# Kernel optimization log

Measured on AMD Instinct MI355X. Metric: run time of the kernel, lower is better.

Reference implementation:

```python
import jax, jax.numpy as jnp
import numpy as np

LAMBDA_DEPTHG = 0.3
STEGO_TEMPERATURE = 0.1
KNN_K = 7
DEPTH_SIGMA = 0.5
EPS = 1e-8


def _l2norm(x):
    return x / jnp.sqrt(jnp.sum(x * x, axis=-1, keepdims=True) + EPS)


def _stego_loss(codes, feats, temperature, knn_k):
    # Pairwise cosine similarity of DINO features -> KNN graph (includes self).
    f = _l2norm(feats)                                  # (B,N,Df)
    sim_f = jnp.einsum('bnd,bmd->bnm', f, f)            # (B,N,N)
    _, knn_idx = jax.lax.top_k(sim_f, knn_k)            # (B,N,k) int32
    # Temperature-scaled InfoNCE over code similarities; KNN entries are positives.
    c = _l2norm(codes)                                  # (B,N,Dc)
    logits = jnp.einsum('bnd,bmd->bnm', c, c) / temperature  # (B,N,N)
    logp = jax.nn.log_softmax(logits, axis=-1)          # (B,N,N)
    pos_logp = jnp.take_along_axis(logp, knn_idx, axis=-1)   # (B,N,k)
    return -jnp.mean(pos_logp)


def _depth_guided_correlation_loss(codes, depth, sigma_d):
    # Gaussian depth affinity: pixels at similar depth should have similar codes.
    dd = depth[:, :, None] - depth[:, None, :]          # (B,N,N)
    w = jnp.exp(-(dd * dd) / (2.0 * sigma_d * sigma_d)) # (B,N,N)
    c = _l2norm(codes)
    s = jnp.einsum('bnd,bmd->bnm', c, c)                # (B,N,N) cosine corr
    return jnp.mean(w * (1.0 - s))


def setup_inputs() -> dict:
    key = jax.random.key(0)
    k1, k2, k3 = jax.random.split(key, 3)
    B, N = 2, 4096
    semantic_codes = jax.random.normal(k1, (B, N, 90), dtype=jnp.float32)
    dino_features = jax.random.normal(k2, (B, N, 384), dtype=jnp.float32)
    depth = jax.random.uniform(k3, (B, N), dtype=jnp.float32)
    return {"semantic_codes": semantic_codes, "dino_features": dino_features, "depth": depth}


def reference(semantic_codes, dino_features, depth):
    l_stego = _stego_loss(semantic_codes, dino_features, STEGO_TEMPERATURE, KNN_K)
    l_depthg = _depth_guided_correlation_loss(semantic_codes, depth, DEPTH_SIGMA)
    total = l_stego + LAMBDA_DEPTHG * l_depthg
    return (l_stego, l_depthg, total)
```

## Files before the change

### kernel.cpp

```cpp
#include <hip/hip_runtime.h>
#include <math.h>

#define NPTS 4096

typedef __attribute__((ext_vector_type(8))) short bf16x8;
typedef __attribute__((ext_vector_type(16))) float f32x16;
typedef long fp8x8;

#define KEEP(x) asm volatile("" : "+v"(x))

__device__ __forceinline__ f32x16 zero16() {
  f32x16 z;
#pragma unroll
  for (int i = 0; i < 16; ++i) z[i] = 0.f;
  return z;
}

__device__ __forceinline__ unsigned packkey(float x, int m) {
  unsigned u = __float_as_uint(x);
  unsigned key = u ^ ((unsigned)((int)u >> 31) | 0x80000000u);
  return (key & 0xFFFFF000u) | (unsigned)m;
}

__device__ __forceinline__ void cas7(unsigned v, unsigned* s) {
#pragma unroll
  for (int t = 0; t < 7; ++t) {
    const unsigned hi = s[t] >= v ? s[t] : v;
    const unsigned lo = s[t] >= v ? v : s[t];
    s[t] = hi;
    v = lo;
  }
}

#define KSENT 0u

__device__ __forceinline__ unsigned bf16pack(float a, float b) {
  unsigned ua = __float_as_uint(a); ua = (ua + 0x7FFFu + ((ua >> 16) & 1u)) >> 16;
  unsigned ub = __float_as_uint(b); ub = (ub + 0x7FFFu + ((ub >> 16) & 1u)) >> 16;
  return ua | (ub << 16);
}

__global__ __launch_bounds__(64) void norm_all(const float* __restrict__ feats,
                                               const float* __restrict__ codes,
                                               unsigned char* __restrict__ Fsw8,
                                               unsigned short* __restrict__ Csw,
                                               float* __restrict__ invc) {
  const int row = blockIdx.x;
  const int lane = threadIdx.x;
  const int b = row >> 12, mt = (row >> 5) & 127, rl = row & 31;

  const float* f = feats + (size_t)row * 384;
  float v[8];
  float ss = 0.f;
  if (lane < 48) {
    float4 p0 = *(const float4*)(f + lane * 8);
    float4 p1 = *(const float4*)(f + lane * 8 + 4);
    v[0] = p0.x; v[1] = p0.y; v[2] = p0.z; v[3] = p0.w;
    v[4] = p1.x; v[5] = p1.y; v[6] = p1.z; v[7] = p1.w;
#pragma unroll
    for (int e = 0; e < 8; ++e) ss = fmaf(v[e], v[e], ss);
  }
#pragma unroll
  for (int m = 1; m <= 32; m <<= 1) ss += __shfl_xor(ss, m, 64);
  const float s8 = rsqrtf(ss + 1e-8f) * 8.0f;
  if (lane < 48) {
    int w0 = __builtin_amdgcn_cvt_pk_fp8_f32(v[0] * s8, v[1] * s8, 0, 0);
    w0 = __builtin_amdgcn_cvt_pk_fp8_f32(v[2] * s8, v[3] * s8, w0, 1);
    int w1 = __builtin_amdgcn_cvt_pk_fp8_f32(v[4] * s8, v[5] * s8, 0, 0);
    w1 = __builtin_amdgcn_cvt_pk_fp8_f32(v[6] * s8, v[7] * s8, w1, 1);
    const int kc = lane >> 1, hs = lane & 1;
    uint2 o = make_uint2((unsigned)w0, (unsigned)w1);
    *(uint2*)(Fsw8 + (((size_t)(b * 128 + mt) * 24 + kc) << 9) + (hs * 32 + rl) * 8) = o;
  }

  const float* c = codes + (size_t)row * 90;
  float cv[8];
#pragma unroll
  for (int e = 0; e < 8; ++e) cv[e] = 0.f;
  if (lane < 11) {
    float4 p0 = *(const float4*)(c + lane * 8);
    float4 p1 = *(const float4*)(c + lane * 8 + 4);
    cv[0] = p0.x; cv[1] = p0.y; cv[2] = p0.z; cv[3] = p0.w;
    cv[4] = p1.x; cv[5] = p1.y; cv[6] = p1.z; cv[7] = p1.w;
  } else if (lane == 11) {
    cv[0] = c[88]; cv[1] = c[89];
  }
  float cs = 0.f;
#pragma unroll
  for (int e = 0; e < 8; ++e) cs = fmaf(cv[e], cv[e], cs);
#pragma unroll
  for (int m = 1; m <= 32; m <<= 1) cs += __shfl_xor(cs, m, 64);
  const float cinv = rsqrtf(cs + 1e-8f);
  if (lane < 12) {
    uint4 o;
    o.x = bf16pack(cv[0] * cinv, cv[1] * cinv);
    o.y = bf16pack(cv[2] * cinv, cv[3] * cinv);
    o.z = bf16pack(cv[4] * cinv, cv[5] * cinv);
    o.w = bf16pack(cv[6] * cinv, cv[7] * cinv);
    const int kc = lane >> 1, hs = lane & 1;
    *(uint4*)(Csw + (((size_t)(b * 128 + mt) * 6 + kc) << 9) + (hs * 32 + rl) * 8) = o;
  }
  if (lane == 0) invc[row] = cinv;
}

__global__ __launch_bounds__(1024, 1) void knn_mfma(const unsigned char* __restrict__ Fsw8,
                                                    unsigned* __restrict__ cand) {
  __shared__ unsigned ckey[16][32][7];
  const int g = blockIdx.x;
  const int b = g & 1;
  const int qt = g >> 1;
  const int q0 = qt * 32;
  const int tid = threadIdx.x;
  const int w = tid >> 6;
  const int lane = tid & 63;
  const int lo = lane & 31, hi4 = (lane >> 5) * 4;
  const unsigned char* Fb = Fsw8 + (size_t)b * 128 * 24 * 512;

  fp8x8 bfr[24];
  {
    const unsigned char* qb = Fb + ((size_t)qt * 24) * 512 + lane * 8;
#pragma unroll
    for (int t = 0; t < 24; ++t) bfr[t] = *(const fp8x8*)(qb + t * 512);
#pragma unroll
    for (int t = 0; t < 24; ++t) KEEP(bfr[t]);
  }
  unsigned s7[7];
#pragma unroll
  for (int t = 0; t < 7; ++t) s7[t] = KSENT;

  const int t0 = w * 8;
  const unsigned char* ab = Fb + ((size_t)t0 * 24) * 512 + lane * 8;

  fp8x8 a[12];
  for (int mt = 0; mt < 8; ++mt) {
    const unsigned char* art = ab + (size_t)mt * 24 * 512;
    f32x16 acc = zero16();
#pragma unroll
    for (int t = 0; t < 12; ++t) a[t] = *(const fp8x8*)(art + t * 512);
#pragma unroll
    for (int t = 0; t < 12; ++t) KEEP(a[t]);
#pragma unroll
    for (int t = 0; t < 12; ++t)
      acc = __builtin_amdgcn_mfma_f32_32x32x16_fp8_fp8(a[t], bfr[t], acc, 0, 0, 0);
#pragma unroll
    for (int t = 0; t < 12; ++t) a[t] = *(const fp8x8*)(art + (12 + t) * 512);
#pragma unroll
    for (int t = 0; t < 12; ++t) KEEP(a[t]);
#pragma unroll
    for (int t = 0; t < 12; ++t)
      acc = __builtin_amdgcn_mfma_f32_32x32x16_fp8_fp8(a[t], bfr[12 + t], acc, 0, 0, 0);
    const int mb = (t0 + mt) * 32 + hi4;
#pragma unroll
    for (int r = 0; r < 16; ++r) {
      const int m = mb + (r & 3) + 8 * (r >> 2);
      cas7(packkey(acc[r], m), s7);
    }
  }

#pragma unroll
  for (int t = 0; t < 7; ++t) {
    const unsigned ov = (unsigned)__shfl_xor((int)s7[t], 32, 64);
    cas7(ov, s7);
  }
  if (lane < 32) {
#pragma unroll
    for (int t = 0; t < 7; ++t) ckey[w][lo][t] = s7[t];
  }
  __syncthreads();

  if (tid < 32) {
    unsigned fs[7];
#pragma unroll
    for (int t = 0; t < 7; ++t) fs[t] = KSENT;
    for (int w2 = 0; w2 < 16; ++w2)
#pragma unroll
      for (int t = 0; t < 7; ++t) cas7(ckey[w2][tid][t], fs);
    unsigned* o = cand + ((size_t)(b * NPTS) + q0 + tid) * 7;
#pragma unroll
    for (int t = 0; t < 7; ++t) o[t] = fs[t];
  }
}

__global__ __launch_bounds__(512, 1) void lse_depth(const unsigned short* __restrict__ Csw,
                                                    const float* __restrict__ depth,
                                                    float* __restrict__ slse_part,
                                                    float* __restrict__ dpart) {
  __shared__ float lsep[8][32];
  __shared__ float depp[8];
  const int g = blockIdx.x;
  const int b = g & 1;
  const int h = (g >> 1) & 1;
  const int qt = g >> 2;
  const int q0 = qt * 32;
  const int tid = threadIdx.x;
  const int w = tid >> 6;
  const int lane = tid & 63;
  const int lo = lane & 31, hi4 = (lane >> 5) * 4;
  const unsigned short* Cb = Csw + (size_t)b * 128 * 6 * 512;
  const float* db = depth + b * NPTS;

  bf16x8 bfr[6];
  {
    const unsigned short* qb = Cb + ((size_t)qt * 6) * 512 + lane * 8;
#pragma unroll
    for (int t = 0; t < 6; ++t) bfr[t] = *(const bf16x8*)(qb + t * 512);
#pragma unroll
    for (int t = 0; t < 6; ++t) KEEP(bfr[t]);
  }
  const float dq = db[q0 + lo];
  float slse = 0.f, sdep = 0.f;

  const int t0 = h * 64 + w * 8;
  const unsigned short* ab = Cb + ((size_t)t0 * 6) * 512 + lane * 8;

  bf16x8 a0[6], a1[6];
#pragma unroll
  for (int t = 0; t < 6; ++t) a0[t] = *(const bf16x8*)(ab + t * 512);
#pragma unroll
  for (int t = 0; t < 6; ++t) KEEP(a0[t]);

#define PROC3(A, GT)                                                           \
  {                                                                            \
    f32x16 acc = zero16();                                                     \
    _Pragma("unroll")                                                          \
    for (int t = 0; t < 6; ++t)                                                \
      acc = __builtin_amdgcn_mfma_f32_32x32x16_bf16(A[t], bfr[t], acc, 0, 0, 0); \
    float dvv[16];                                                             \
    _Pragma("unroll")                                                          \
    for (int k = 0; k < 4; ++k) {                                              \
      float4 dv = *(const float4*)(db + (GT) * 32 + hi4 + 8 * k);              \
      dvv[k * 4 + 0] = dv.x; dvv[k * 4 + 1] = dv.y;                            \
      dvv[k * 4 + 2] = dv.z; dvv[k * 4 + 3] = dv.w;                            \
    }                                                                          \
    _Pragma("unroll")                                                          \
    for (int r = 0; r < 16; ++r) {                                             \
      const float s = acc[r];                                                  \
      const float dd = dq - dvv[r];                                            \
      sdep += __expf(-2.f * dd * dd) * (1.f - s);                              \
      slse += __expf(fmaf(s, 10.f, -10.f));                                    \
    }                                                                          \
  }

  for (int mt = 0; mt < 8; mt += 2) {
    {
      const unsigned short* ar = ab + (size_t)(mt + 1) * 6 * 512;
#pragma unroll
      for (int t = 0; t < 6; ++t) a1[t] = *(const bf16x8*)(ar + t * 512);
#pragma unroll
      for (int t = 0; t < 6; ++t) KEEP(a1[t]);
    }
    PROC3(a0, t0 + mt)
    if (mt + 2 < 8) {
      const unsigned short* ar = ab + (size_t)(mt + 2) * 6 * 512;
#pragma unroll
      for (int t = 0; t < 6; ++t) a0[t] = *(const bf16x8*)(ar + t * 512);
#pragma unroll
      for (int t = 0; t < 6; ++t) KEEP(a0[t]);
    }
    PROC3(a1, t0 + mt + 1)
  }
#undef PROC3

  slse += __shfl_xor(slse, 32, 64);
  if (lane < 32) lsep[w][lo] = slse;
#pragma unroll
  for (int m = 1; m <= 32; m <<= 1) sdep += __shfl_xor(sdep, m, 64);
  if (lane == 0) depp[w] = sdep;
  __syncthreads();
  if (tid < 32) {
    float tot = 0.f;
#pragma unroll
    for (int w2 = 0; w2 < 8; ++w2) tot += lsep[w2][tid];
    slse_part[(size_t)((h * 2 + b) * NPTS) + q0 + tid] = tot;
  }
  if (tid == 32) {
    float d = 0.f;
#pragma unroll
    for (int w2 = 0; w2 < 8; ++w2) d += depp[w2];
    dpart[g] = d;
  }
}

__global__ __launch_bounds__(64) void gather_pos(const float* __restrict__ codes,
                                                 const float* __restrict__ invc,
                                                 const unsigned* __restrict__ cand,
                                                 float* __restrict__ gpart) {
  const int n = blockIdx.x;
  const int b = n >> 12, q = n & 4095;
  const int lane = threadIdx.x;

  unsigned s[7];
  const unsigned* cp = cand + (size_t)n * 7;
#pragma unroll
  for (int t = 0; t < 7; ++t) s[t] = cp[t];
  bool has = false;
#pragma unroll
  for (int t = 0; t < 7; ++t) has = has || ((s[t] & 4095u) == (unsigned)q);
  if (!has) s[6] = (unsigned)q;

  const float* cn = codes + (size_t)n * 90;
  float2 a = make_float2(0.f, 0.f);
  if (lane < 45) a = *(const float2*)(cn + lane * 2);
  const float inva = invc[n];
  float ssum = 0.f;
#pragma unroll
  for (int k = 0; k < 7; ++k) {
    const int m = (int)(s[k] & 4095u);
    const float* cm = codes + ((size_t)(b << 12) + m) * 90;
    float2 bb = make_float2(0.f, 0.f);
    if (lane < 45) bb = *(const float2*)(cm + lane * 2);
    float p = fmaf(a.x, bb.x, a.y * bb.y);
#pragma unroll
    for (int w = 1; w <= 32; w <<= 1) p += __shfl_xor(p, w, 64);
    ssum += p * inva * invc[(b << 12) + m];
  }
  if (lane == 0) gpart[n] = ssum;
}

__global__ __launch_bounds__(256) void finalize(const float* __restrict__ slse_part,
                                                const float* __restrict__ gpart,
                                                const float* __restrict__ dpart,
                                                float* __restrict__ out) {
  const int tid = threadIdx.x;
  float s1 = 0.f, s2 = 0.f;
  for (int n = tid; n < 2 * NPTS; n += 256) {
    const int b = n >> 12, q = n & 4095;
    const float pz = slse_part[b * NPTS + q] + slse_part[(2 + b) * NPTS + q];
    s1 += 10.f + __logf(pz);
    s2 += gpart[n];
  }
  float s3 = dpart[tid] + dpart[tid + 256];
  __shared__ float r1[256], r2[256], r3[256];
  r1[tid] = s1; r2[tid] = s2; r3[tid] = s3;
  __syncthreads();
  for (int s = 128; s > 0; s >>= 1) {
    if (tid < s) { r1[tid] += r1[tid + s]; r2[tid] += r2[tid + s]; r3[tid] += r3[tid + s]; }
    __syncthreads();
  }
  if (tid == 0) {
    const float l_st = (7.f * r1[0] - 10.f * r2[0]) / 57344.f;
    const float l_dp = r3[0] / 33554432.f;
    out[0] = l_st;
    out[1] = l_dp;
    out[2] = l_st + 0.3f * l_dp;
  }
}

extern "C" void kernel_launch(void* const* d_in, const int* in_sizes, int n_in,
                              void* d_out, int out_size, void* d_ws, size_t ws_size,
                              hipStream_t stream) {
  (void)in_sizes; (void)n_in; (void)out_size; (void)ws_size;
  const float* codes = (const float*)d_in[0];
  const float* feats = (const float*)d_in[1];
  const float* depth = (const float*)d_in[2];
  float* out = (float*)d_out;

  char* ws = (char*)d_ws;
  float*    invc      = (float*)ws;
  unsigned* cand      = (unsigned*)(ws + 32768);
  unsigned char*  Fsw8 = (unsigned char*)(ws + 262144);
  unsigned short* Csw  = (unsigned short*)(ws + 3407872);
  float*    slse_part = (float*)(ws + 4980736);
  float*    dpart     = (float*)(ws + 5046272);
  float*    gpart     = (float*)(ws + 5048320);

  norm_all<<<2 * NPTS, 64, 0, stream>>>(feats, codes, Fsw8, Csw, invc);
  knn_mfma<<<256, 1024, 0, stream>>>(Fsw8, cand);
  lse_depth<<<512, 512, 0, stream>>>(Csw, depth, slse_part, dpart);
  gather_pos<<<2 * NPTS, 64, 0, stream>>>(codes, invc, cand, gpart);
  finalize<<<1, 256, 0, stream>>>(slse_part, gpart, dpart, out);
}
```

Before: 89.76 us.

## Stage KNN query fragments in LDS, double-buffer key loads, merge LSE halves

In the KNN kernel the 24 query fp8 fragments now go into shared memory instead of staying pinned in registers, and the key-tile loads are double-buffered so the next tile's first half is fetched while the current MFMAs run. This frees VGPRs and hides global load latency, at the cost of LDS reads on every iteration. Separately, lse_depth now runs 1024 threads per block across all 128 key tiles, so each query's full sum is done in one block and the log is taken there. That removes the split-half partials and simplifies finalize, but halves the grid to 256 blocks.

```diff
diff --git a/kernel.cpp b/kernel.cpp
--- a/kernel.cpp
+++ b/kernel.cpp
@@ -105,6 +105,7 @@
 
 __global__ __launch_bounds__(1024, 1) void knn_mfma(const unsigned char* __restrict__ Fsw8,
                                                     unsigned* __restrict__ cand) {
+  __shared__ unsigned long long qfrag[24 * 64];
   __shared__ unsigned ckey[16][32][7];
   const int g = blockIdx.x;
   const int b = g & 1;
@@ -116,14 +117,17 @@
   const int lo = lane & 31, hi4 = (lane >> 5) * 4;
   const unsigned char* Fb = Fsw8 + (size_t)b * 128 * 24 * 512;
 
-  fp8x8 bfr[24];
   {
-    const unsigned char* qb = Fb + ((size_t)qt * 24) * 512 + lane * 8;
-#pragma unroll
-    for (int t = 0; t < 24; ++t) bfr[t] = *(const fp8x8*)(qb + t * 512);
-#pragma unroll
-    for (int t = 0; t < 24; ++t) KEEP(bfr[t]);
-  }
+    const unsigned long long* src =
+        (const unsigned long long*)(Fb + ((size_t)qt * 24) * 512);
+#pragma unroll
+    for (int k = 0; k < 2; ++k) {
+      const int i = tid + k * 1024;
+      if (i < 24 * 64) qfrag[i] = src[i];
+    }
+  }
+  __syncthreads();
+
   unsigned s7[7];
 #pragma unroll
   for (int t = 0; t < 7; ++t) s7[t] = KSENT;
@@ -131,24 +135,40 @@
   const int t0 = w * 8;
   const unsigned char* ab = Fb + ((size_t)t0 * 24) * 512 + lane * 8;
 
-  fp8x8 a[12];
+  fp8x8 a0[12], a1[12], bq[12];
+#pragma unroll
+  for (int t = 0; t < 12; ++t) a0[t] = *(const fp8x8*)(ab + t * 512);
+#pragma unroll
+  for (int t = 0; t < 12; ++t) KEEP(a0[t]);
+
   for (int mt = 0; mt < 8; ++mt) {
     const unsigned char* art = ab + (size_t)mt * 24 * 512;
+#pragma unroll
+    for (int t = 0; t < 12; ++t) a1[t] = *(const fp8x8*)(art + (12 + t) * 512);
+#pragma unroll
+    for (int t = 0; t < 12; ++t) KEEP(a1[t]);
+#pragma unroll
+    for (int t = 0; t < 12; ++t) bq[t] = (fp8x8)qfrag[t * 64 + lane];
+#pragma unroll
+    for (int t = 0; t < 12; ++t) KEEP(bq[t]);
     f32x16 acc = zero16();
 #pragma unroll
-    for (int t = 0; t < 12; ++t) a[t] = *(const fp8x8*)(art + t * 512);
-#pragma unroll
-    for (int t = 0; t < 12; ++t) KEEP(a[t]);
-#pragma unroll
     for (int t = 0; t < 12; ++t)
-      acc = __builtin_amdgcn_mfma_f32_32x32x16_fp8_fp8(a[t], bfr[t], acc, 0, 0, 0);
-#pragma unroll
-    for (int t = 0; t < 12; ++t) a[t] = *(const fp8x8*)(art + (12 + t) * 512);
-#pragma unroll
-    for (int t = 0; t < 12; ++t) KEEP(a[t]);
+      acc = __builtin_amdgcn_mfma_f32_32x32x16_fp8_fp8(a0[t], bq[t], acc, 0, 0, 0);
+    if (mt + 1 < 8) {
+      const unsigned char* arn = ab + (size_t)(mt + 1) * 24 * 512;
+#pragma unroll
+      for (int t = 0; t < 12; ++t) a0[t] = *(const fp8x8*)(arn + t * 512);
+#pragma unroll
+      for (int t = 0; t < 12; ++t) KEEP(a0[t]);
+    }
+#pragma unroll
+    for (int t = 0; t < 12; ++t) bq[t] = (fp8x8)qfrag[(12 + t) * 64 + lane];
+#pragma unroll
+    for (int t = 0; t < 12; ++t) KEEP(bq[t]);
 #pragma unroll
     for (int t = 0; t < 12; ++t)
-      acc = __builtin_amdgcn_mfma_f32_32x32x16_fp8_fp8(a[t], bfr[12 + t], acc, 0, 0, 0);
+      acc = __builtin_amdgcn_mfma_f32_32x32x16_fp8_fp8(a1[t], bq[t], acc, 0, 0, 0);
     const int mb = (t0 + mt) * 32 + hi4;
 #pragma unroll
     for (int r = 0; r < 16; ++r) {
@@ -181,16 +201,15 @@
   }
 }
 
-__global__ __launch_bounds__(512, 1) void lse_depth(const unsigned short* __restrict__ Csw,
-                                                    const float* __restrict__ depth,
-                                                    float* __restrict__ slse_part,
-                                                    float* __restrict__ dpart) {
-  __shared__ float lsep[8][32];
-  __shared__ float depp[8];
+__global__ __launch_bounds__(1024, 1) void lse_depth(const unsigned short* __restrict__ Csw,
+                                                     const float* __restrict__ depth,
+                                                     float* __restrict__ lse_out,
+                                                     float* __restrict__ dpart) {
+  __shared__ float lsep[16][32];
+  __shared__ float depp[16];
   const int g = blockIdx.x;
   const int b = g & 1;
-  const int h = (g >> 1) & 1;
-  const int qt = g >> 2;
+  const int qt = g >> 1;
   const int q0 = qt * 32;
   const int tid = threadIdx.x;
   const int w = tid >> 6;
@@ -210,7 +229,7 @@
   const float dq = db[q0 + lo];
   float slse = 0.f, sdep = 0.f;
 
-  const int t0 = h * 64 + w * 8;
+  const int t0 = w * 8;
   const unsigned short* ab = Cb + ((size_t)t0 * 6) * 512 + lane * 8;
 
   bf16x8 a0[6], a1[6];
@@ -270,13 +289,13 @@
   if (tid < 32) {
     float tot = 0.f;
 #pragma unroll
-    for (int w2 = 0; w2 < 8; ++w2) tot += lsep[w2][tid];
-    slse_part[(size_t)((h * 2 + b) * NPTS) + q0 + tid] = tot;
+    for (int w2 = 0; w2 < 16; ++w2) tot += lsep[w2][tid];
+    lse_out[(size_t)(b * NPTS) + q0 + tid] = 10.f + __logf(tot);
   }
   if (tid == 32) {
     float d = 0.f;
 #pragma unroll
-    for (int w2 = 0; w2 < 8; ++w2) d += depp[w2];
+    for (int w2 = 0; w2 < 16; ++w2) d += depp[w2];
     dpart[g] = d;
   }
 }
@@ -317,19 +336,17 @@
   if (lane == 0) gpart[n] = ssum;
 }
 
-__global__ __launch_bounds__(256) void finalize(const float* __restrict__ slse_part,
+__global__ __launch_bounds__(256) void finalize(const float* __restrict__ lse_out,
                                                 const float* __restrict__ gpart,
                                                 const float* __restrict__ dpart,
                                                 float* __restrict__ out) {
   const int tid = threadIdx.x;
   float s1 = 0.f, s2 = 0.f;
   for (int n = tid; n < 2 * NPTS; n += 256) {
-    const int b = n >> 12, q = n & 4095;
-    const float pz = slse_part[b * NPTS + q] + slse_part[(2 + b) * NPTS + q];
-    s1 += 10.f + __logf(pz);
+    s1 += lse_out[n];
     s2 += gpart[n];
   }
-  float s3 = dpart[tid] + dpart[tid + 256];
+  float s3 = dpart[tid];
   __shared__ float r1[256], r2[256], r3[256];
   r1[tid] = s1; r2[tid] = s2; r3[tid] = s3;
   __syncthreads();
@@ -360,13 +377,13 @@
   unsigned* cand      = (unsigned*)(ws + 32768);
   unsigned char*  Fsw8 = (unsigned char*)(ws + 262144);
   unsigned short* Csw  = (unsigned short*)(ws + 3407872);
-  float*    slse_part = (float*)(ws + 4980736);
-  float*    dpart     = (float*)(ws + 5046272);
-  float*    gpart     = (float*)(ws + 5048320);
+  float*    lse_out   = (float*)(ws + 4980736);
+  float*    dpart     = (float*)(ws + 5013504);
+  float*    gpart     = (float*)(ws + 5014528);
 
   norm_all<<<2 * NPTS, 64, 0, stream>>>(feats, codes, Fsw8, Csw, invc);
   knn_mfma<<<256, 1024, 0, stream>>>(Fsw8, cand);
-  lse_depth<<<512, 512, 0, stream>>>(Csw, depth, slse_part, dpart);
+  lse_depth<<<256, 1024, 0, stream>>>(Csw, depth, lse_out, dpart);
   gather_pos<<<2 * NPTS, 64, 0, stream>>>(codes, invc, cand, gpart);
-  finalize<<<1, 256, 0, stream>>>(slse_part, gpart, dpart, out);
-}
+  finalize<<<1, 256, 0, stream>>>(lse_out, gpart, dpart, out);
+}
```

New measurement: 88.79 us. Within noise of the previous version (-1.1%).
